# Performance work log

Hardware: AMD Instinct MI355X
Metric: run time of the kernel (lower is better)

## Reference

```python
import jax, jax.numpy as jnp
import numpy as np
import math

B, C, W, H = 4, 64, 128, 128
S = 2                 # len(shifts)
SHIFTS = (1, 2)       # dilations
HC = C // S           # hidden_channels = 32
NL = 8                # num_layer (8 diff stencils)
AREA = W * H
EPS = 1e-5


def _base_kernels():
    # 4 forward diff stencils + their 180-degree flips (delta2 = delta1[:, :, ::-1, ::-1])
    d1 = np.array([[[-1, 0, 0], [0, 1, 0], [0, 0, 0]],
                   [[0, -1, 0], [0, 1, 0], [0, 0, 0]],
                   [[0, 0, -1], [0, 1, 0], [0, 0, 0]],
                   [[0, 0, 0], [0, 1, -1], [0, 0, 0]]], dtype=np.float32).reshape(4, 1, 3, 3)
    d2 = d1[:, :, ::-1, ::-1].copy()
    return np.concatenate([d1, d2], axis=0)  # (8, 1, 3, 3)

# Depthwise kernel: per input channel, all 8 stencils (feature_group_count=HC layout)
_DW_KERNEL = jnp.asarray(np.tile(_base_kernels()[None], (HC, 1, 1, 1, 1)).reshape(NL * HC, 1, 3, 3))


def setup_inputs() -> dict:
    key = jax.random.key(0)
    ks = jax.random.split(key, 6)
    s = 0.05
    return {
        "x": jax.random.normal(ks[0], (B, C, W, H), jnp.float32),
        "trans_w": jax.random.normal(ks[1], (C, C), jnp.float32) * s,
        "bn1_g": jnp.ones((C,), jnp.float32),
        "bn1_b": jnp.zeros((C,), jnp.float32),
        "query_w": jax.random.normal(ks[2], (S, HC, HC), jnp.float32) * s,
        "key_w": jax.random.normal(ks[3], (S, (NL + 1) * HC, (NL + 1) * HC), jnp.float32) * s,
        "out_w": jax.random.normal(ks[4], (C, C), jnp.float32) * s,
        "bn2_g": jnp.ones((C,), jnp.float32),
        "bn2_b": jnp.zeros((C,), jnp.float32),
    }


def _bn_relu(y, g, b):
    # train-mode BatchNorm2d (biased batch stats) + ReLU
    m = y.mean((0, 2, 3), keepdims=True)
    v = y.var((0, 2, 3), keepdims=True)
    return jax.nn.relu((y - m) * jax.lax.rsqrt(v + EPS) * g[None, :, None, None] + b[None, :, None, None])


def _dw_diff_convs(x, dil):
    # x: (B, HC, W, H) -> 8 depthwise dilated 3x3 diff convs, concat order kernel-major
    y = jax.lax.conv_general_dilated(
        x, _DW_KERNEL, window_strides=(1, 1), padding='SAME',
        rhs_dilation=(dil, dil), feature_group_count=HC,
        dimension_numbers=('NCHW', 'OIHW', 'NCHW'))
    # grouped layout is (channel, stencil); torch concat order is (stencil, channel)
    return y.reshape(B, HC, NL, W, H).transpose(0, 2, 1, 3, 4).reshape(B, NL * HC, W, H)


def _inorm(w):
    # InstanceNorm2d(affine=False) over the last two dims, per (batch, shift)
    m = w.mean((-2, -1), keepdims=True)
    v = w.var((-2, -1), keepdims=True)
    return (w - m) * jax.lax.rsqrt(v + EPS)


def _l2n(x):
    # F.normalize(dim=-1)
    n = jnp.linalg.norm(x, axis=-1, keepdims=True)
    return x / jnp.maximum(n, 1e-12)


def reference(x, trans_w, bn1_g, bn1_b, query_w, key_w, out_w, bn2_g, bn2_b):
    y = _bn_relu(jnp.einsum('bchw,oc->bohw', x, trans_w), bn1_g, bn1_b)
    cens = y.reshape(B, S, HC, W, H)  # torch.chunk along channels
    keys, qrys, svs = [], [], []
    for i in range(S):
        c = cens[:, i]
        sur = _dw_diff_convs(c, SHIFTS[i])                                      # (B, 8*HC, W, H)
        kk = jnp.einsum('bchw,oc->bohw', jnp.concatenate([sur, c], 1), key_w[i])
        qq = jnp.einsum('bchw,oc->bohw', c, query_w[i])
        keys.append(kk.reshape(B, (NL + 1) * HC, AREA))
        qrys.append(qq.reshape(B, HC, AREA))
        svs.append(sur.reshape(B, NL * HC, AREA))
    keys = _l2n(jnp.stack(keys, 1))     # (B, S, 9*HC, AREA)
    qrys = _l2n(jnp.stack(qrys, 1))     # (B, S, HC, AREA)
    svs = jnp.stack(svs, 1)             # (B, S, 8*HC, AREA)
    w = jnp.einsum('bsca,bska->bsck', qrys, keys) / math.sqrt(AREA)  # (B, S, HC, 9*HC)
    sw = jax.nn.softmax(_inorm(w[..., :NL * HC]), axis=-1)           # (B, S, HC, 8*HC)
    out = jnp.einsum('bsck,bska->bsca', sw, svs).reshape(B, C, W, H)
    return _bn_relu(jnp.einsum('bchw,oc->bohw', out, out_w), bn2_g, bn2_b)
```

## Files before the change

kernel.cpp:

```cpp
#include <hip/hip_runtime.h>

#define BB 4
#define CC 64
#define SS 2
#define HCC 32
#define AREA_ 16384
#define KDIM 288
#define YPITCH 44

typedef _Float16 half8 __attribute__((ext_vector_type(8)));
typedef float f32x16 __attribute__((ext_vector_type(16)));

static __device__ __forceinline__ float warp_rsum(float v){
#pragma unroll
  for (int o=32;o>0;o>>=1) v += __shfl_down(v,o,64);
  return v;
}
static __device__ __forceinline__ float warp_rmax(float v){
#pragma unroll
  for (int o=32;o>0;o>>=1) v = fmaxf(v,__shfl_down(v,o,64));
  return v;
}

__global__ __launch_bounds__(256) void conv64_kernel(const float* __restrict__ in,
    const float* __restrict__ wmat, float* __restrict__ out){
  int b = blockIdx.x >> 7;
  int p0 = (blockIdx.x & 127) << 7;
  __shared__ float tile[64][132];
  __shared__ float wsm[64][68];
  for (int idx = threadIdx.x; idx < 4096; idx += 256){
    int c = idx & 63, o = idx >> 6;
    wsm[c][o] = wmat[o*64 + c];
  }
  const float* inb = in + (size_t)b*CC*AREA_ + p0;
  for (int idx = threadIdx.x; idx < 8192; idx += 256){
    int c = idx >> 7, pp = idx & 127;
    tile[c][pp] = inb[(size_t)c*AREA_ + pp];
  }
  __syncthreads();
  int px = (threadIdx.x & 31) * 4;
  int og = threadIdx.x >> 5;
  float4 acc[8];
#pragma unroll
  for (int i=0;i<8;i++) acc[i] = make_float4(0.f,0.f,0.f,0.f);
  for (int c=0;c<64;c++){
    float4 v  = *(const float4*)&tile[c][px];
    float4 w0 = *(const float4*)&wsm[c][og*8];
    float4 w1 = *(const float4*)&wsm[c][og*8+4];
    float wv[8] = {w0.x,w0.y,w0.z,w0.w,w1.x,w1.y,w1.z,w1.w};
#pragma unroll
    for (int i=0;i<8;i++){
      acc[i].x = fmaf(wv[i], v.x, acc[i].x);
      acc[i].y = fmaf(wv[i], v.y, acc[i].y);
      acc[i].z = fmaf(wv[i], v.z, acc[i].z);
      acc[i].w = fmaf(wv[i], v.w, acc[i].w);
    }
  }
  float* ob = out + (size_t)b*CC*AREA_ + p0 + px;
#pragma unroll
  for (int i=0;i<8;i++)
    *(float4*)&ob[(size_t)(og*8+i)*AREA_] = acc[i];
}

__global__ __launch_bounds__(256) void bn_part_kernel(const float* __restrict__ src,
    float* __restrict__ part){
  int c = blockIdx.x, chunk = blockIdx.y;
  float s1=0.f, s2=0.f;
  for (int b=0;b<BB;b++){
    const float* p = src + ((size_t)b*CC + c)*AREA_ + chunk*2048;
    for (int i=threadIdx.x;i<2048;i+=256){ float v=p[i]; s1+=v; s2+=v*v; }
  }
  __shared__ float red[8];
  float w1 = warp_rsum(s1), w2 = warp_rsum(s2);
  int lane = threadIdx.x & 63, wid = threadIdx.x >> 6;
  if (lane==0){ red[wid]=w1; red[4+wid]=w2; }
  __syncthreads();
  if (threadIdx.x==0){
    atomicAdd(&part[c], red[0]+red[1]+red[2]+red[3]);
    atomicAdd(&part[64+c], red[4]+red[5]+red[6]+red[7]);
  }
}

__global__ void bn_fin_kernel(const float* __restrict__ part, const float* __restrict__ gam,
    const float* __restrict__ bet, float* __restrict__ sb){
  int c = threadIdx.x;
  const float N = (float)(BB*AREA_);
  float m = part[c]/N;
  float var = part[64+c]/N - m*m;
  float sc = gam[c]*rsqrtf(var + 1e-5f);
  sb[c] = sc;
  sb[64+c] = bet[c] - m*sc;
}

__global__ __launch_bounds__(256) void bn_apply_relu_kernel(const float* __restrict__ src,
    const float* __restrict__ sb, float* __restrict__ dst){
  size_t i = (size_t)blockIdx.x*256 + threadIdx.x;
  int c = (int)((i >> 14) & 63);
  float v = fmaf(src[i], sb[c], sb[64+c]);
  dst[i] = v > 0.f ? v : 0.f;
}

__global__ __launch_bounds__(256) void qq_kernel(const float* __restrict__ y,
    const float* __restrict__ qw, float* __restrict__ qq){
  int blk = blockIdx.x;
  int p0 = (blk & 127) << 7;
  int s = (blk >> 7) & 1;
  int b = blk >> 8;
  __shared__ float tile[32][132];
  __shared__ float wsm[32][36];
  const float* qws = qw + s*HCC*HCC;
  for (int idx=threadIdx.x; idx<1024; idx+=256){
    int c = idx & 31, o = idx >> 5;
    wsm[c][o] = qws[o*32 + c];
  }
  const float* yb = y + ((size_t)b*CC + s*HCC)*AREA_ + p0;
  for (int idx=threadIdx.x; idx<4096; idx+=256){
    int c=idx>>7, pp=idx&127;
    tile[c][pp] = yb[(size_t)c*AREA_ + pp];
  }
  __syncthreads();
  int px = (threadIdx.x & 31) * 4;
  int og = threadIdx.x >> 5;
  float4 acc[4];
#pragma unroll
  for (int i=0;i<4;i++) acc[i] = make_float4(0.f,0.f,0.f,0.f);
  for (int c=0;c<32;c++){
    float4 v  = *(const float4*)&tile[c][px];
    float4 w0 = *(const float4*)&wsm[c][og*4];
    float wv[4] = {w0.x,w0.y,w0.z,w0.w};
#pragma unroll
    for (int i=0;i<4;i++){
      acc[i].x = fmaf(wv[i], v.x, acc[i].x);
      acc[i].y = fmaf(wv[i], v.y, acc[i].y);
      acc[i].z = fmaf(wv[i], v.z, acc[i].z);
      acc[i].w = fmaf(wv[i], v.w, acc[i].w);
    }
  }
  float* ob = qq + ((size_t)(b*SS+s)*HCC)*AREA_ + p0 + px;
#pragma unroll
  for (int i=0;i<4;i++)
    *(float4*)&ob[(size_t)(og*4+i)*AREA_] = acc[i];
}

__global__ __launch_bounds__(256,2) void gram_kernel(const float* __restrict__ y,
    const float* __restrict__ qq, float* __restrict__ dpart, float* __restrict__ wpart){
  const int PAarr[6]={0,0,1,0,1,2}, PBarr[6]={0,1,1,2,2,2};
  int bid = blockIdx.x;
  int bs = bid & 7;
  int slot = 67 - (bid >> 3);
  int pair, Kstart, nch;
  if (slot < 48){ pair = slot>>4; Kstart = (slot&15)<<10; nch=16; }
  else if (slot < 64){ pair = 3 + ((slot-48)>>3); Kstart = ((slot-48)&7)<<11; nch=32; }
  else { pair=5; Kstart = (slot-64)<<12; nch=64; }
  int PA = PAarr[pair], PB = PBarr[pair];
  int RA = PA<2?128:64, CB = PB<2?128:64;
  bool diag = (PA==PB);
  int rows_tot = RA + (diag?0:CB);
  int passes = rows_tot >> 5;
  int s = bs & 1, b = bs >> 1, dil = 1+s;
  const float* yb = y + ((size_t)b*CC + s*HCC)*AREA_;
  const float* qqb = qq + (size_t)bs*HCC*AREA_;
  __shared__ __align__(16) _Float16 Us[256*64];
  int tid = threadIdx.x;
  int hq = tid & 7, rr8 = tid >> 3;
  int lane = tid & 63, wid = tid >> 6;
  int rbase = (wid>>1)*64, cbase = (wid&1)*64;
  bool active = (rbase < RA) && (cbase < CB);
  int boff = diag ? 0 : RA;
  int r0 = rbase + (lane&31), r1 = r0+32;
  int cr0 = boff + cbase + (lane&31), cr1 = cr0+32;
  int uo = lane>>5;

  auto loadPass = [&](int t, int p)->half8{
    int k0 = Kstart + t*64;
    int w = k0>>7, h = (k0&127) + hq*8;
    int pr = p*32 + rr8;
    int pan, prow;
    if (pr < RA){ pan = PA; prow = pr; } else { pan = PB; prow = pr - RA; }
    float vv[8];
    if (pan < 2){
      int l = pan*4 + (prow>>5), ch = prow & 31;
      int oy = ((0x6A40 >> (2*l)) & 3) - 1;
      int ox = ((0x6A4  >> (2*l)) & 3) - 1;
      const float* crow = yb + (size_t)ch*AREA_ + w*128 + h;
      float4 ca = *(const float4*)crow;
      float4 cb = *(const float4*)(crow+4);
      float cen[8] = {ca.x,ca.y,ca.z,ca.w,cb.x,cb.y,cb.z,cb.w};
      float nb[8];
      int wy = w + oy*dil, oxd = ox*dil, hb = h + oxd;
      if (wy>=0 && wy<128){
        const float* nrow = yb + (size_t)ch*AREA_ + wy*128 + hb;
        if (hb>=0 && hb<=120){
          float4 na, nc;
          __builtin_memcpy(&na, nrow, 16);
          __builtin_memcpy(&nc, nrow+4, 16);
          nb[0]=na.x; nb[1]=na.y; nb[2]=na.z; nb[3]=na.w;
          nb[4]=nc.x; nb[5]=nc.y; nb[6]=nc.z; nb[7]=nc.w;
        } else {
#pragma unroll
          for (int j=0;j<8;j++){
            int hx = hb + j;
            nb[j] = (hx>=0 && hx<128) ? nrow[j] : 0.f;
          }
        }
      } else {
#pragma unroll
        for (int j=0;j<8;j++) nb[j]=0.f;
      }
#pragma unroll
      for (int j=0;j<8;j++) vv[j] = cen[j]-nb[j];
    } else {
      const float* src = (prow<32) ? yb + (size_t)prow*AREA_ : qqb + (size_t)(prow-32)*AREA_;
      const float* crow = src + w*128 + h;
      float4 ca = *(const float4*)crow;
      float4 cb = *(const float4*)(crow+4);
      vv[0]=ca.x; vv[1]=ca.y; vv[2]=ca.z; vv[3]=ca.w;
      vv[4]=cb.x; vv[5]=cb.y; vv[6]=cb.z; vv[7]=cb.w;
    }
    half8 hv;
#pragma unroll
    for (int j=0;j<8;j++) hv[j] = (_Float16)vv[j];
    return hv;
  };
  auto writeLDS = [&](int p, half8 hv){
    int pr = p*32 + rr8;
    *(half8*)&Us[(size_t)pr*64 + ((hq ^ (pr&7))<<3)] = hv;
  };

  bool p4 = (passes >= 4), p6 = (passes >= 6), p8 = (passes >= 8);
  half8 f0{}, f1{}, f2{}, f3{}, f4{}, f5{}, f6{}, f7{};

  f32x16 acc00={}, acc01={}, acc10={}, acc11={};
  f0 = loadPass(0,0); f1 = loadPass(0,1);
  if (p4){ f2 = loadPass(0,2); f3 = loadPass(0,3); }
  if (p6){ f4 = loadPass(0,4); f5 = loadPass(0,5); }
  if (p8){ f6 = loadPass(0,6); f7 = loadPass(0,7); }
  for (int t=0; t<nch; ++t){
    asm volatile("s_waitcnt lgkmcnt(0)" ::: "memory");
    __builtin_amdgcn_s_barrier();
    writeLDS(0,f0); writeLDS(1,f1);
    if (p4){ writeLDS(2,f2); writeLDS(3,f3); }
    if (p6){ writeLDS(4,f4); writeLDS(5,f5); }
    if (p8){ writeLDS(6,f6); writeLDS(7,f7); }
    if (t+1 < nch){
      f0 = loadPass(t+1,0); f1 = loadPass(t+1,1);
      if (p4){ f2 = loadPass(t+1,2); f3 = loadPass(t+1,3); }
      if (p6){ f4 = loadPass(t+1,4); f5 = loadPass(t+1,5); }
      if (p8){ f6 = loadPass(t+1,6); f7 = loadPass(t+1,7); }
    }
    asm volatile("s_waitcnt lgkmcnt(0)" ::: "memory");
    __builtin_amdgcn_s_barrier();
    if (active){
#pragma unroll
      for (int st=0; st<4; ++st){
        int u = st*2 + uo;
        half8 a0 = *(const half8*)&Us[(size_t)r0*64  + ((u^(r0&7))<<3)];
        half8 a1 = *(const half8*)&Us[(size_t)r1*64  + ((u^(r1&7))<<3)];
        half8 b0 = *(const half8*)&Us[(size_t)cr0*64 + ((u^(cr0&7))<<3)];
        half8 b1 = *(const half8*)&Us[(size_t)cr1*64 + ((u^(cr1&7))<<3)];
        acc00 = __builtin_amdgcn_mfma_f32_32x32x16_f16(a0,b0,acc00,0,0,0);
        acc01 = __builtin_amdgcn_mfma_f32_32x32x16_f16(a0,b1,acc01,0,0,0);
        acc10 = __builtin_amdgcn_mfma_f32_32x32x16_f16(a1,b0,acc10,0,0,0);
        acc11 = __builtin_amdgcn_mfma_f32_32x32x16_f16(a1,b1,acc11,0,0,0);
      }
    }
  }
  if (active){
    int gid = bs*68 + slot;
    float* pp = (gid<256)? dpart + (size_t)gid*16384 : wpart + (size_t)(gid-256)*16384;
    int rr = 4*uo, cc = lane&31;
#pragma unroll
    for (int reg=0;reg<16;reg++){
      int ro = (reg&3) + 8*(reg>>2) + rr;
      pp[(size_t)(rbase+ro)*128 + cbase+cc]       = acc00[reg];
      pp[(size_t)(rbase+ro)*128 + cbase+32+cc]    = acc01[reg];
      pp[(size_t)(rbase+32+ro)*128 + cbase+cc]    = acc10[reg];
      pp[(size_t)(rbase+32+ro)*128 + cbase+32+cc] = acc11[reg];
    }
  }
}

__global__ __launch_bounds__(256) void reduce_kernel(const float* __restrict__ dpart,
    const float* __restrict__ wpart, float* __restrict__ P){
  const int PAarr[6]={0,0,1,0,1,2}, PBarr[6]={0,1,1,2,2,2};
  const int slotbase[6]={0,16,32,48,56,64}, nkarr[6]={16,16,16,8,8,4};
  const int chunkbase[7]={0,16,32,48,56,64,68};
  int chunk = blockIdx.x, bs = blockIdx.y;
  int pair = 0;
  while (chunk >= chunkbase[pair+1]) pair++;
  int lc = chunk - chunkbase[pair];
  int PA = PAarr[pair], PB = PBarr[pair];
  int CN = PB<2?128:64;
  int Roff = PA*128, Coff = PB*128;
  int nk = nkarr[pair], sb0 = slotbase[pair];
  int csh = (CN==128)?7:6;
  int cell0 = lc*1024 + threadIdx.x*4;
  int r = cell0 >> csh, c = cell0 & (CN-1);
  float4 v = make_float4(0.f,0.f,0.f,0.f);
  int gidb = bs*68 + sb0;
  for (int k=0;k<nk;k++){
    int gid = gidb + k;
    const float* pp = (gid<256)? dpart + (size_t)gid*16384 : wpart + (size_t)(gid-256)*16384;
    float4 t = *(const float4*)&pp[(size_t)r*128 + c];
    v.x += t.x; v.y += t.y; v.z += t.z; v.w += t.w;
  }
  float* Pb = P + (size_t)bs*102400;
  *(float4*)&Pb[(size_t)(Roff+r)*320 + Coff+c] = v;
  Pb[(size_t)(Coff+c  )*320 + Roff+r] = v.x;
  Pb[(size_t)(Coff+c+1)*320 + Roff+r] = v.y;
  Pb[(size_t)(Coff+c+2)*320 + Roff+r] = v.z;
  Pb[(size_t)(Coff+c+3)*320 + Roff+r] = v.w;
}

__global__ __launch_bounds__(256) void kwT_kernel(const float* __restrict__ kw, float* __restrict__ kwT){
  int idx = blockIdx.x*256 + threadIdx.x;
  if (idx >= 2*KDIM*KDIM) return;
  int s = idx / (KDIM*KDIM);
  int r = idx - s*KDIM*KDIM;
  int k = r / KDIM, j = r - k*KDIM;
  kwT[(size_t)s*KDIM*KDIM + (size_t)j*KDIM + k] = kw[idx];
}

__global__ __launch_bounds__(256) void vknorm_kernel(const float* __restrict__ P,
    const float* __restrict__ kwT, float* __restrict__ kn){
  int j = blockIdx.x, bs = blockIdx.y;
  int s = bs & 1;
  __shared__ float prow[KDIM];
  const float* Pb = P + (size_t)bs*102400 + (size_t)j*320;
  for (int i=threadIdx.x;i<KDIM;i+=256) prow[i]=Pb[i];
  __syncthreads();
  const float* kt = kwT + (size_t)s*KDIM*KDIM;
  int k = threadIdx.x;
  float acc=0.f;
  for (int jp=0;jp<KDIM;jp++) acc = fmaf(prow[jp], kt[(size_t)jp*KDIM + k], acc);
  atomicAdd(&kn[bs*256 + k], kt[(size_t)j*KDIM + k] * acc);
}

__global__ __launch_bounds__(256) void wmat_kernel(const float* __restrict__ P,
    const float* __restrict__ kwT, const float* __restrict__ kn,
    float* __restrict__ wbuf, float* __restrict__ wstats){
  int bs = blockIdx.x >> 5, c = blockIdx.x & 31;
  int s = bs & 1;
  __shared__ float prow[KDIM];
  const float* PbB = P + (size_t)bs*102400;
  const float* Pb = PbB + (size_t)(288+c)*320;
  for (int i=threadIdx.x;i<KDIM;i+=256) prow[i]=Pb[i];
  __syncthreads();
  const float* kt = kwT + (size_t)s*KDIM*KDIM;
  int k = threadIdx.x;
  float acc=0.f;
  for (int j=0;j<KDIM;j++) acc = fmaf(prow[j], kt[(size_t)j*KDIM + k], acc);
  float rk = 1.f/fmaxf(sqrtf(fmaxf(kn[bs*256+k],0.f)),1e-12f);
  float qn = PbB[(size_t)(288+c)*320 + 288+c];
  float rq = 1.f/fmaxf(sqrtf(fmaxf(qn,0.f)),1e-12f);
  float wv = acc * rq * rk * (1.f/128.f);
  wbuf[((size_t)bs*32 + c)*256 + k] = wv;
  __shared__ float red[8];
  float r1 = warp_rsum(wv), r2 = warp_rsum(wv*wv);
  int lane = threadIdx.x & 63, wid = threadIdx.x >> 6;
  if (lane==0){ red[wid]=r1; red[4+wid]=r2; }
  __syncthreads();
  if (threadIdx.x==0){
    atomicAdd(&wstats[bs*2],   red[0]+red[1]+red[2]+red[3]);
    atomicAdd(&wstats[bs*2+1], red[4]+red[5]+red[6]+red[7]);
  }
}

__global__ __launch_bounds__(256) void smx_kernel(const float* __restrict__ wbuf,
    const float* __restrict__ wstats, float* __restrict__ sw){
  int bs = blockIdx.x >> 5, c = blockIdx.x & 31;
  float s1 = wstats[bs*2], s2 = wstats[bs*2+1];
  const float N = 8192.f;
  float m = s1/N, var = s2/N - m*m;
  float rs = rsqrtf(var + 1e-5f);
  int k = threadIdx.x;
  float v = (wbuf[((size_t)bs*32 + c)*256 + k] - m)*rs;
  __shared__ float red[4];
  float mx = warp_rmax(v);
  int lane = k & 63, wid = k >> 6;
  if (lane==0) red[wid]=mx;
  __syncthreads();
  float MX = fmaxf(fmaxf(red[0],red[1]),fmaxf(red[2],red[3]));
  __syncthreads();
  float e = expf(v - MX);
  float es = warp_rsum(e);
  if (lane==0) red[wid]=es;
  __syncthreads();
  float ES = red[0]+red[1]+red[2]+red[3];
  sw[((size_t)bs*32 + c)*256 + k] = e/ES;
}

__global__ __launch_bounds__(256) void tswf_kernel(const float* __restrict__ sw, _Float16* __restrict__ tswf){
  int idx = blockIdx.x*256 + threadIdx.x;
  if (idx >= 9216) return;
  int lane = idx & 63;
  int ks = (idx >> 6) % 18;
  int bs = idx / (18*64);
  int c = lane & 31;
  const float* swb = sw + ((size_t)bs*32 + c)*256;
  half8 hv;
#pragma unroll
  for (int j=0;j<8;j++){
    int k = ks*16 + ((lane>>5)<<3) + j;
    int t = k >> 5, ch = k & 31;
    float v;
    if (t==0){ v=0.f; for (int l=0;l<8;l++) v += swb[l*32+ch]; }
    else v = -swb[(t-1)*32 + ch];
    hv[j] = (_Float16)v;
  }
  *(half8*)&tswf[(size_t)idx*8] = hv;
}

__global__ __launch_bounds__(256,2) void attn_mfma_kernel(const float* __restrict__ y,
    const _Float16* __restrict__ tswf, float* __restrict__ outs){
  int blk = blockIdx.x;
  int w = blk & 127;
  int s = (blk >> 7) & 1;
  int b = blk >> 8;
  int bs = b*SS + s;
  int dil = 1 + s;
  __shared__ __align__(16) _Float16 ybuf[3*132*YPITCH];
  const float* yb = y + ((size_t)bs*HCC)*AREA_;
  int tid = threadIdx.x;
  int lane = tid & 63, wid = tid >> 6;

  const _Float16* tf = tswf + ((size_t)bs*18*64 + lane)*8;
  half8 afr[18];
#pragma unroll
  for (int ks=0; ks<18; ++ks) afr[ks] = *(const half8*)&tf[(size_t)ks*64*8];

  for (int i = tid; i < 384; i += 256){
    int ch = i & 31;
    int q = i >> 5;
    int wr = q >> 2, hb = q & 3;
    int hi = (hb < 2) ? hb : (128 + hb);
    int oct = (ch>>3) ^ ((hi>>2)&3);
    ybuf[(size_t)(wr*132+hi)*YPITCH + oct*8 + (ch&7)] = (_Float16)0.f;
  }
  int ch8 = tid >> 5;
  int h4 = (tid & 31) * 4;
#pragma unroll
  for (int r = 0; r < 12; ++r){
    int wr = r >> 2, chg = r & 3;
    int wy = w + (wr-1)*dil;
    if (wy < 0 || wy >= 128) continue;
    int ch = chg*8 + ch8;
    float4 v = *(const float4*)&yb[(size_t)ch*AREA_ + wy*128 + h4];
    float vv[4] = {v.x, v.y, v.z, v.w};
#pragma unroll
    for (int j=0;j<4;j++){
      int hi = h4 + 2 + j;
      int oct = (ch>>3) ^ ((hi>>2)&3);
      ybuf[(size_t)(wr*132+hi)*YPITCH + oct*8 + (ch&7)] = (_Float16)vv[j];
    }
  }
  __syncthreads();

  const int offy[9]={0,-1,-1,-1,0,1,1,1,0};
  const int offx[9]={0,-1,0,1,1,1,0,-1,-1};
  int n0 = wid * 32;
  int nl = n0 + (lane & 31);
  int ko = lane >> 5;
  f32x16 acc = {};
#pragma unroll
  for (int ks=0; ks<18; ++ks){
    int t = ks >> 1;
    int wy = w + offy[t]*dil;
    half8 bfr = {};
    if (wy >= 0 && wy < 128){
      int wr = offy[t] + 1;
      int hi = nl + offx[t]*dil + 2;
      int oct = (((ks&1)<<1) | ko) ^ ((hi>>2)&3);
      bfr = *(const half8*)&ybuf[(size_t)(wr*132+hi)*YPITCH + oct*8];
    }
    acc = __builtin_amdgcn_mfma_f32_32x32x16_f16(afr[ks], bfr, acc, 0,0,0);
  }
  float* ob = outs + (size_t)bs*HCC*AREA_ + (size_t)w*128;
  int col = n0 + (lane & 31);
  int rb = 4*(lane>>5);
#pragma unroll
  for (int reg=0; reg<16; ++reg){
    int c = (reg&3) + 8*(reg>>2) + rb;
    ob[(size_t)c*AREA_ + col] = acc[reg];
  }
}

extern "C" void kernel_launch(void* const* d_in, const int* in_sizes, int n_in,
                              void* d_out, int out_size, void* d_ws, size_t ws_size,
                              hipStream_t stream){
  const float* x   = (const float*)d_in[0];
  const float* tw  = (const float*)d_in[1];
  const float* g1  = (const float*)d_in[2];
  const float* b1  = (const float*)d_in[3];
  const float* qw  = (const float*)d_in[4];
  const float* kw  = (const float*)d_in[5];
  const float* ow  = (const float*)d_in[6];
  const float* g2  = (const float*)d_in[7];
  const float* b2  = (const float*)d_in[8];
  float* out = (float*)d_out;
  float* ws = (float*)d_ws;

  float* y      = ws + 64;
  float* qqb    = ws + 4194368;
  float* kwT    = qqb;
  float* wbuf   = ws + 4360256;
  float* wpart  = ws + 8388672;
  float* outs   = wpart;
  float* P      = ws + 13107264;
  float* stats  = ws + 13926464;
  float* wstats = ws + 13926720;
  float* kn     = ws + 13926976;
  float* sb     = ws + 13929024;
  float* swb    = ws + 13929280;
  _Float16* tswf = (_Float16*)(ws + 13994816);
  float* dpart  = (float*)d_out;
  float* z      = y;

  hipMemsetAsync(stats, 0, 2560*sizeof(float), stream);

  conv64_kernel<<<512,256,0,stream>>>(x, tw, y);
  bn_part_kernel<<<dim3(64,8),256,0,stream>>>(y, stats);
  bn_fin_kernel<<<1,64,0,stream>>>(stats, g1, b1, sb);
  bn_apply_relu_kernel<<<16384,256,0,stream>>>(y, sb, y);
  qq_kernel<<<1024,256,0,stream>>>(y, qw, qqb);
  gram_kernel<<<544,256,0,stream>>>(y, qqb, dpart, wpart);
  reduce_kernel<<<dim3(68,8),256,0,stream>>>(dpart, wpart, P);
  kwT_kernel<<<648,256,0,stream>>>(kw, kwT);
  vknorm_kernel<<<dim3(288,8),256,0,stream>>>(P, kwT, kn);
  wmat_kernel<<<256,256,0,stream>>>(P, kwT, kn, wbuf, wstats);
  smx_kernel<<<256,256,0,stream>>>(wbuf, wstats, swb);
  tswf_kernel<<<36,256,0,stream>>>(swb, tswf);
  attn_mfma_kernel<<<1024,256,0,stream>>>(y, tswf, outs);
  conv64_kernel<<<512,256,0,stream>>>(outs, ow, z);
  bn_part_kernel<<<dim3(64,8),256,0,stream>>>(z, stats+128);
  bn_fin_kernel<<<1,64,0,stream>>>(stats+128, g2, b2, sb+128);
  bn_apply_relu_kernel<<<16384,256,0,stream>>>(z, sb+128, out);
}
```

Baseline: 259.6 us.

## Fuse BN statistics into conv, rebalance gram work slots, reorder attention blocks

Batch-norm sum and sum-of-squares are now computed inside the 1x1 conv kernel from the accumulators, with a wave-level shuffle reduction followed by atomics. This removes two separate passes over the activations. The gram kernel now gives every pair uniform 16-chunk K slots (768 blocks) with compact partial tiles and a higher occupancy hint, and the reduce kernel is updated to match. Attention blocks are reindexed so neighbouring blocks cover different batch/shift pairs. The cost is more atomics per conv block and more partial tiles for the reduce to sum.

```diff
diff --git a/kernel.cpp b/kernel.cpp
--- a/kernel.cpp
+++ b/kernel.cpp
@@ -23,7 +23,7 @@
 }
 
 __global__ __launch_bounds__(256) void conv64_kernel(const float* __restrict__ in,
-    const float* __restrict__ wmat, float* __restrict__ out){
+    const float* __restrict__ wmat, float* __restrict__ out, float* __restrict__ part){
   int b = blockIdx.x >> 7;
   int p0 = (blockIdx.x & 127) << 7;
   __shared__ float tile[64][132];
@@ -60,24 +60,26 @@
 #pragma unroll
   for (int i=0;i<8;i++)
     *(float4*)&ob[(size_t)(og*8+i)*AREA_] = acc[i];
-}
-
-__global__ __launch_bounds__(256) void bn_part_kernel(const float* __restrict__ src,
-    float* __restrict__ part){
-  int c = blockIdx.x, chunk = blockIdx.y;
-  float s1=0.f, s2=0.f;
-  for (int b=0;b<BB;b++){
-    const float* p = src + ((size_t)b*CC + c)*AREA_ + chunk*2048;
-    for (int i=threadIdx.x;i<2048;i+=256){ float v=p[i]; s1+=v; s2+=v*v; }
-  }
-  __shared__ float red[8];
-  float w1 = warp_rsum(s1), w2 = warp_rsum(s2);
-  int lane = threadIdx.x & 63, wid = threadIdx.x >> 6;
-  if (lane==0){ red[wid]=w1; red[4+wid]=w2; }
-  __syncthreads();
-  if (threadIdx.x==0){
-    atomicAdd(&part[c], red[0]+red[1]+red[2]+red[3]);
-    atomicAdd(&part[64+c], red[4]+red[5]+red[6]+red[7]);
+  float s1[8], s2[8];
+#pragma unroll
+  for (int i=0;i<8;i++){
+    s1[i] = acc[i].x+acc[i].y+acc[i].z+acc[i].w;
+    s2[i] = acc[i].x*acc[i].x+acc[i].y*acc[i].y+acc[i].z*acc[i].z+acc[i].w*acc[i].w;
+  }
+#pragma unroll
+  for (int o=16;o>0;o>>=1){
+#pragma unroll
+    for (int i=0;i<8;i++){
+      s1[i] += __shfl_down(s1[i], o, 32);
+      s2[i] += __shfl_down(s2[i], o, 32);
+    }
+  }
+  if ((threadIdx.x & 31) == 0){
+#pragma unroll
+    for (int i=0;i<8;i++){
+      atomicAdd(&part[og*8+i], s1[i]);
+      atomicAdd(&part[64+og*8+i], s2[i]);
+    }
   }
 }
 
@@ -142,16 +144,19 @@
     *(float4*)&ob[(size_t)(og*4+i)*AREA_] = acc[i];
 }
 
-__global__ __launch_bounds__(256,2) void gram_kernel(const float* __restrict__ y,
+__global__ __launch_bounds__(256,4) void gram_kernel(const float* __restrict__ y,
     const float* __restrict__ qq, float* __restrict__ dpart, float* __restrict__ wpart){
   const int PAarr[6]={0,0,1,0,1,2}, PBarr[6]={0,1,1,2,2,2};
+  const int pairOrder[6]={1,3,4,0,2,5};
+  const int pairbase[6]={0,262144,524288,786432,917504,1048576};
+  const int tsz[6]={16384,16384,16384,8192,8192,4096};
   int bid = blockIdx.x;
   int bs = bid & 7;
-  int slot = 67 - (bid >> 3);
-  int pair, Kstart, nch;
-  if (slot < 48){ pair = slot>>4; Kstart = (slot&15)<<10; nch=16; }
-  else if (slot < 64){ pair = 3 + ((slot-48)>>3); Kstart = ((slot-48)&7)<<11; nch=32; }
-  else { pair=5; Kstart = (slot-64)<<12; nch=64; }
+  int sidx = bid >> 3;
+  int pair = pairOrder[sidx >> 4];
+  int slotIdx = sidx & 15;
+  int Kstart = slotIdx << 10;
+  const int nch = 16;
   int PA = PAarr[pair], PB = PBarr[pair];
   int RA = PA<2?128:64, CB = PB<2?128:64;
   bool diag = (PA==PB);
@@ -266,16 +271,17 @@
     }
   }
   if (active){
-    int gid = bs*68 + slot;
-    float* pp = (gid<256)? dpart + (size_t)gid*16384 : wpart + (size_t)(gid-256)*16384;
+    size_t off = (size_t)bs*1114112 + pairbase[pair] + (size_t)slotIdx*tsz[pair];
+    float* pp = (off < 4194304) ? (dpart + off) : (wpart + (off - 4194304));
+    int cp = (pair<3)?128:64;
     int rr = 4*uo, cc = lane&31;
 #pragma unroll
     for (int reg=0;reg<16;reg++){
       int ro = (reg&3) + 8*(reg>>2) + rr;
-      pp[(size_t)(rbase+ro)*128 + cbase+cc]       = acc00[reg];
-      pp[(size_t)(rbase+ro)*128 + cbase+32+cc]    = acc01[reg];
-      pp[(size_t)(rbase+32+ro)*128 + cbase+cc]    = acc10[reg];
-      pp[(size_t)(rbase+32+ro)*128 + cbase+32+cc] = acc11[reg];
+      pp[(size_t)(rbase+ro)*cp + cbase+cc]       = acc00[reg];
+      pp[(size_t)(rbase+ro)*cp + cbase+32+cc]    = acc01[reg];
+      pp[(size_t)(rbase+32+ro)*cp + cbase+cc]    = acc10[reg];
+      pp[(size_t)(rbase+32+ro)*cp + cbase+32+cc] = acc11[reg];
     }
   }
 }
@@ -283,25 +289,24 @@
 __global__ __launch_bounds__(256) void reduce_kernel(const float* __restrict__ dpart,
     const float* __restrict__ wpart, float* __restrict__ P){
   const int PAarr[6]={0,0,1,0,1,2}, PBarr[6]={0,1,1,2,2,2};
-  const int slotbase[6]={0,16,32,48,56,64}, nkarr[6]={16,16,16,8,8,4};
+  const int pairbase[6]={0,262144,524288,786432,917504,1048576};
+  const int tsz[6]={16384,16384,16384,8192,8192,4096};
   const int chunkbase[7]={0,16,32,48,56,64,68};
   int chunk = blockIdx.x, bs = blockIdx.y;
   int pair = 0;
   while (chunk >= chunkbase[pair+1]) pair++;
   int lc = chunk - chunkbase[pair];
-  int PA = PAarr[pair], PB = PBarr[pair];
-  int CN = PB<2?128:64;
-  int Roff = PA*128, Coff = PB*128;
-  int nk = nkarr[pair], sb0 = slotbase[pair];
+  int CN = (pair<3)?128:64;
+  int Roff = PAarr[pair]*128, Coff = PBarr[pair]*128;
   int csh = (CN==128)?7:6;
   int cell0 = lc*1024 + threadIdx.x*4;
   int r = cell0 >> csh, c = cell0 & (CN-1);
   float4 v = make_float4(0.f,0.f,0.f,0.f);
-  int gidb = bs*68 + sb0;
-  for (int k=0;k<nk;k++){
-    int gid = gidb + k;
-    const float* pp = (gid<256)? dpart + (size_t)gid*16384 : wpart + (size_t)(gid-256)*16384;
-    float4 t = *(const float4*)&pp[(size_t)r*128 + c];
+  size_t base = (size_t)bs*1114112 + pairbase[pair];
+  for (int k=0;k<16;k++){
+    size_t off = base + (size_t)k*tsz[pair];
+    const float* pp = (off < 4194304) ? (dpart + off) : (wpart + (off - 4194304));
+    float4 t = *(const float4*)&pp[(size_t)r*CN + c];
     v.x += t.x; v.y += t.y; v.z += t.z; v.w += t.w;
   }
   float* Pb = P + (size_t)bs*102400;
@@ -414,10 +419,9 @@
 __global__ __launch_bounds__(256,2) void attn_mfma_kernel(const float* __restrict__ y,
     const _Float16* __restrict__ tswf, float* __restrict__ outs){
   int blk = blockIdx.x;
-  int w = blk & 127;
-  int s = (blk >> 7) & 1;
-  int b = blk >> 8;
-  int bs = b*SS + s;
+  int bs = blk & 7;
+  int w = blk >> 3;
+  int s = bs & 1;
   int dil = 1 + s;
   __shared__ __align__(16) _Float16 ybuf[3*132*YPITCH];
   const float* yb = y + ((size_t)bs*HCC)*AREA_;
@@ -518,12 +522,11 @@
 
   hipMemsetAsync(stats, 0, 2560*sizeof(float), stream);
 
-  conv64_kernel<<<512,256,0,stream>>>(x, tw, y);
-  bn_part_kernel<<<dim3(64,8),256,0,stream>>>(y, stats);
+  conv64_kernel<<<512,256,0,stream>>>(x, tw, y, stats);
   bn_fin_kernel<<<1,64,0,stream>>>(stats, g1, b1, sb);
   bn_apply_relu_kernel<<<16384,256,0,stream>>>(y, sb, y);
   qq_kernel<<<1024,256,0,stream>>>(y, qw, qqb);
-  gram_kernel<<<544,256,0,stream>>>(y, qqb, dpart, wpart);
+  gram_kernel<<<768,256,0,stream>>>(y, qqb, dpart, wpart);
   reduce_kernel<<<dim3(68,8),256,0,stream>>>(dpart, wpart, P);
   kwT_kernel<<<648,256,0,stream>>>(kw, kwT);
   vknorm_kernel<<<dim3(288,8),256,0,stream>>>(P, kwT, kn);
@@ -531,8 +534,7 @@
   smx_kernel<<<256,256,0,stream>>>(wbuf, wstats, swb);
   tswf_kernel<<<36,256,0,stream>>>(swb, tswf);
   attn_mfma_kernel<<<1024,256,0,stream>>>(y, tswf, outs);
-  conv64_kernel<<<512,256,0,stream>>>(outs, ow, z);
-  bn_part_kernel<<<dim3(64,8),256,0,stream>>>(z, stats+128);
+  conv64_kernel<<<512,256,0,stream>>>(outs, ow, z, stats+128);
   bn_fin_kernel<<<1,64,0,stream>>>(stats+128, g2, b2, sb+128);
   bn_apply_relu_kernel<<<16384,256,0,stream>>>(z, sb+128, out);
 }
```

Result: slower. 503.5 us (+94.0%).
